# Kernel optimization log

Measured on AMD Instinct MI355X. Metric: run time of the kernel, lower is better.

Reference implementation:

```python
import jax, jax.numpy as jnp
import numpy as np

NUM_NODES = 100
WINDOW = 128
GH = 256       # graph_hidden_channels
DH = 64        # discrepancy_hidden_channels
OUT = 128      # out_channels
B = 256        # graphs per batch
N = B * NUM_NODES
E = 409600


def _mconv(x, w, b):
    # x: [B, n, W], w: [n, 2, k], b: [n, 2]  (per-node Conv1d(1,2,k), 'same' padding)
    k = w.shape[-1]
    W = x.shape[-1]
    p = k // 2
    xp = jnp.pad(x, ((0, 0), (0, 0), (p, p)))
    win = jnp.stack([xp[..., j:j + W] for j in range(k)], axis=-1)  # [B,n,W,k]
    return jnp.einsum('bnwk,nck->bncw', win, w) + b[None, :, :, None]


def _gcn(x, edge_index, Wg, bg):
    # PyG GCNConv: add self-loops, symmetric normalization, then linear
    Nn = x.shape[0]
    xw = x @ Wg.T
    loops = jnp.arange(Nn, dtype=edge_index.dtype)
    src = jnp.concatenate([edge_index[0], loops])
    dst = jnp.concatenate([edge_index[1], loops])
    deg = jax.ops.segment_sum(jnp.ones(src.shape[0], dtype=xw.dtype), dst, num_segments=Nn)
    norm = jax.lax.rsqrt(jnp.maximum(deg, 1e-12))
    coef = norm[src] * norm[dst]
    agg = jax.ops.segment_sum(coef[:, None] * xw[src], dst, num_segments=Nn)
    return agg + bg


def setup_inputs() -> dict:
    key = jax.random.key(0)
    ks = jax.random.split(key, 20)
    f = 6 * WINDOW
    s = lambda d: 1.0 / np.sqrt(d)
    inp = {
        'x1': jax.random.normal(ks[0], (N, WINDOW), jnp.float32),
        'x2': jax.random.normal(ks[1], (N, WINDOW), jnp.float32),
        'edge_index1': jax.random.randint(ks[2], (2, E), 0, N, jnp.int32),
        'edge_index2': jax.random.randint(ks[3], (2, E), 0, N, jnp.int32),
        'w3': jax.random.normal(ks[4], (NUM_NODES, 2, 3), jnp.float32) * s(3),
        'b3': jax.random.normal(ks[5], (NUM_NODES, 2), jnp.float32) * s(3),
        'w5': jax.random.normal(ks[6], (NUM_NODES, 2, 5), jnp.float32) * s(5),
        'b5': jax.random.normal(ks[7], (NUM_NODES, 2), jnp.float32) * s(5),
        'w7': jax.random.normal(ks[8], (NUM_NODES, 2, 7), jnp.float32) * s(7),
        'b7': jax.random.normal(ks[9], (NUM_NODES, 2), jnp.float32) * s(7),
        'Wff': jax.random.normal(ks[10], (NUM_NODES, GH, f), jnp.float32) * s(f),
        'bff': jax.random.normal(ks[11], (NUM_NODES, GH), jnp.float32) * s(f),
        'Wg': jax.random.normal(ks[12], (GH, GH), jnp.float32) * s(GH),
        'bg': jax.random.normal(ks[13], (GH,), jnp.float32) * s(GH),
        'Wd': jax.random.normal(ks[14], (NUM_NODES, DH, 2 * GH), jnp.float32) * s(2 * GH),
        'bd': jax.random.normal(ks[15], (NUM_NODES, DH), jnp.float32) * s(2 * GH),
        'Wfc': jax.random.normal(ks[16], (OUT, NUM_NODES * DH), jnp.float32) * s(NUM_NODES * DH),
        'bfc': jax.random.normal(ks[17], (OUT,), jnp.float32) * s(NUM_NODES * DH),
    }
    return inp


def reference(x1, x2, edge_index1, edge_index2, w3, b3, w5, b5, w7, b7,
              Wff, bff, Wg, bg, Wd, bd, Wfc, bfc):
    n = w3.shape[0]
    Nn, W = x1.shape
    Bg = Nn // n

    def branch(x):
        xg = x.reshape(Bg, n, W)
        # multiscale CNN: concat conv3/conv5/conv7 along channel -> [B,n,6,W]
        c = jnp.concatenate([_mconv(xg, w3, b3), _mconv(xg, w5, b5), _mconv(xg, w7, b7)], axis=2)
        c = jax.nn.relu(c.reshape(Bg, n, 6 * W))            # channel-major flatten (matches view(-1))
        h = jax.nn.relu(jnp.einsum('bnf,nhf->bnh', c, Wff) + bff)
        return h.reshape(Nn, -1)

    h1 = jax.nn.relu(_gcn(branch(x1), edge_index1, Wg, bg))
    h2 = jax.nn.relu(_gcn(branch(x2), edge_index2, Wg, bg))
    H = h1.shape[-1]
    cat = jnp.concatenate([h1.reshape(Bg, n, H), h2.reshape(Bg, n, H)], axis=-1)  # [B,n,2H]
    d = jnp.einsum('bnf,ndf->bnd', cat, Wd) + bd            # per-node discrepancy FC
    du = jax.nn.relu(d.reshape(Bg, -1))                     # node-major -> [B, n*DH]
    return du @ Wfc.T + bfc
```

## Files before the change

### kernel.cpp

```cpp
#include <hip/hip_runtime.h>

#define DI __device__ __forceinline__

typedef __bf16 bf16_t;
typedef bf16_t bf16x8 __attribute__((ext_vector_type(8)));
typedef float f32x4 __attribute__((ext_vector_type(4)));
typedef ushort ushort8v __attribute__((ext_vector_type(8)));

static constexpr int NNODE = 100, WIN = 128, GH = 256, DH = 64, OUTC = 128, NB = 256;
static constexpr int NTOT = NB * NNODE;
static constexpr int NE = 409600;
static constexpr int FFK = 6 * WIN;
static constexpr size_t CB = (size_t)NNODE * NB * FFK;
static constexpr size_t HB = (size_t)NTOT * GH;
static constexpr int CVT_BLKS = 4064;
static constexpr int NSEG = 64, SEGE = NE / NSEG;
static constexpr int NPK = NTOT / 2;
static constexpr int NRANGE = 4, RDST = NTOT / NRANGE;
static constexpr int RPK = RDST / 2;
static constexpr int HIST_BLKS = 2 * NSEG * NRANGE;

DI ushort f2bf(float f) {
  union { float f; unsigned u; } v; v.f = f;
  unsigned r = v.u + 0x7fffu + ((v.u >> 16) & 1u);
  return (ushort)(r >> 16);
}
DI float bf2f(ushort s) {
  union { unsigned u; float f; } v; v.u = ((unsigned)s) << 16; return v.f;
}
DI float u2f(uint u) { union { uint u; float f; } v; v.u = u; return v.f; }

DI void gload16(const void* g, void* l) {
  __builtin_amdgcn_global_load_lds((const __attribute__((address_space(1))) void*)g,
                                   (__attribute__((address_space(3))) void*)l, 16, 0, 0);
}


DI void cvt_body(int bx, const float* s0, const float* s1, const float* s2,
                 ushort* d0, ushort* d1, ushort* d2) {
  int j = bx * 256 + threadIdx.x;
  const float* s; ushort* d;
  if (j < 3276800 / 4) { s = s0; d = d0; }
  else if ((j -= 3276800 / 4) < 819200 / 4) { s = s1; d = d1; }
  else { j -= 819200 / 4; s = s2; d = d2; }
  float4 v = reinterpret_cast<const float4*>(s)[j];
  ushort4 o;
  o.x = f2bf(v.x); o.y = f2bf(v.y); o.z = f2bf(v.z); o.w = f2bf(v.w);
  reinterpret_cast<ushort4*>(d)[j] = o;
}

DI void histseg_body(int bx, const int* e1d, const int* e2d,
                     ushort* rank_local, uint* segcnt, uint* cnt ) {
  int set = bx & 1, seg = (bx >> 1) & (NSEG - 1), range = bx >> 7;
  int tid = threadIdx.x;
  for (int k = tid; k < RPK; k += 256) cnt[k] = 0;
  __syncthreads();
  const int* dstp = (set ? e2d : e1d) + seg * SEGE;
  ushort* rl = rank_local + set * NE + seg * SEGE;
  const int dbase = range * RDST;
#pragma unroll
  for (int k = 0; k < SEGE / 256; ++k) {
    int i = k * 256 + tid;
    uint dl = (uint)(dstp[i] - dbase);
    if (dl < (uint)RDST) {
      uint sh = (dl & 1) * 16;
      uint old = atomicAdd(&cnt[dl >> 1], 1u << sh);
      rl[i] = (ushort)((old >> sh) & 0xffffu);
    }
  }
  __syncthreads();
  uint* sc = segcnt + (size_t)(set * NSEG + seg) * NPK + range * RPK;
  for (int k = tid; k < RPK; k += 256) sc[k] = cnt[k];
}

DI void fill_body(int bx, const int* e1, const int* e2, const int* offs,
                  const ushort* rank_local, const uint* segbase, int* csr) {
  int i = bx * 256 + threadIdx.x;
  int set = i >= NE;
  int ii = i - set * NE;
  const int* e = set ? e2 : e1;
  int d = e[NE + ii];
  int seg = ii / SEGE;
  uint b32 = segbase[(size_t)(set * NSEG + seg) * NPK + (d >> 1)];
  int base = (b32 >> ((d & 1) * 16)) & 0xffff;
  int pos = offs[set * (NTOT + 1) + d] + base + rank_local[i];
  csr[set * NE + pos] = e[ii];
}

DI void segscan_body(int set, int pb, const uint* segcnt, uint* segbase, int* deg) {
  int p = pb * 256 + threadIdx.x;
  uint lo = 0, hi = 0;
  const uint* sc = segcnt + (size_t)set * NSEG * NPK + p;
  uint* sb = segbase + (size_t)set * NSEG * NPK + p;
  for (int s = 0; s < NSEG; ++s) {
    uint v = sc[(size_t)s * NPK];
    sb[(size_t)s * NPK] = lo | (hi << 16);
    lo += v & 0xffffu; hi += v >> 16;
  }
  reinterpret_cast<int2*>(deg)[set * NPK + p] = make_int2((int)lo, (int)hi);
}

DI void scan_body(int set, const int* deg_, int* offs_, float* norm_) {
  const int* deg = deg_ + set * NTOT;
  int* offs = offs_ + set * (NTOT + 1);
  float* norm = norm_ + set * NTOT;
  __shared__ int part[256];
  int t = threadIdx.x;
  int base = t * 100;
  int s = 0;
  for (int j = 0; j < 100; ++j) s += deg[base + j];
  part[t] = s;
  __syncthreads();
  for (int d = 1; d < 256; d <<= 1) {
    int vv = (t >= d) ? part[t - d] : 0;
    __syncthreads();
    part[t] += vv;
    __syncthreads();
  }
  int run = (t > 0) ? part[t - 1] : 0;
  for (int j = 0; j < 100; ++j) {
    int dv = deg[base + j];
    offs[base + j] = run;
    norm[base + j] = rsqrtf((float)(dv + 1));
    run += dv;
  }
  if (t == 255) offs[NTOT] = part[255];
}

DI void conv_body(int bx, const float* x1, const float* x2,
                  const float* w3, const float* b3, const float* w5, const float* b5,
                  const float* w7, const float* b7, ushort* c, float* xs ) {
  const int t = threadIdx.x;
  const int rowi = t >> 4;
  const int idx = t & 15;
  int r = bx * 16 + rowi;
  int br = r >= NTOT;
  int rr = r - br * NTOT;
  const float* x = br ? x2 : x1;
  int b = rr / 100, node = rr - b * 100;

  float* row = xs + rowi * 136;
  const int w0 = idx * 8;
  float4 v0 = *reinterpret_cast<const float4*>(x + (size_t)rr * WIN + w0);
  float4 v1 = *reinterpret_cast<const float4*>(x + (size_t)rr * WIN + w0 + 4);
  *reinterpret_cast<float4*>(&row[4 + w0]) = v0;
  *reinterpret_cast<float4*>(&row[4 + w0 + 4]) = v1;
  if (idx == 0) { row[0] = 0.f; row[1] = 0.f; row[2] = 0.f; row[3] = 0.f; }
  if (idx == 15) { row[132] = 0.f; row[133] = 0.f; row[134] = 0.f; row[135] = 0.f; }
  __syncthreads();

  float xv[14];
#pragma unroll
  for (int j = 0; j < 14; ++j) xv[j] = row[1 + w0 + j];

  const float* W3 = w3 + node * 6;  const float* B3 = b3 + node * 2;
  const float* W5 = w5 + node * 10; const float* B5 = b5 + node * 2;
  const float* W7 = w7 + node * 14; const float* B7 = b7 + node * 2;
  ushort* out = c + (size_t)br * CB + (size_t)(node * NB + b) * FFK + w0;

#pragma unroll
  for (int ch = 0; ch < 2; ++ch) {
    float k3[3], k5[5], k7[7];
#pragma unroll
    for (int j = 0; j < 3; ++j) k3[j] = W3[ch * 3 + j];
#pragma unroll
    for (int j = 0; j < 5; ++j) k5[j] = W5[ch * 5 + j];
#pragma unroll
    for (int j = 0; j < 7; ++j) k7[j] = W7[ch * 7 + j];
    float bb3 = B3[ch], bb5 = B5[ch], bb7 = B7[ch];
    ushort8v o3, o5, o7;
#pragma unroll
    for (int p = 0; p < 8; ++p) {
      float a3 = bb3, a5 = bb5, a7 = bb7;
#pragma unroll
      for (int j = 0; j < 3; ++j) a3 += k3[j] * xv[p + 2 + j];
#pragma unroll
      for (int j = 0; j < 5; ++j) a5 += k5[j] * xv[p + 1 + j];
#pragma unroll
      for (int j = 0; j < 7; ++j) a7 += k7[j] * xv[p + j];
      o3[p] = f2bf(fmaxf(a3, 0.f));
      o5[p] = f2bf(fmaxf(a5, 0.f));
      o7[p] = f2bf(fmaxf(a7, 0.f));
    }
    *reinterpret_cast<ushort8v*>(out + (0 + ch) * WIN) = o3;
    *reinterpret_cast<ushort8v*>(out + (2 + ch) * WIN) = o5;
    *reinterpret_cast<ushort8v*>(out + (4 + ch) * WIN) = o7;
  }
}

template <int MODE>
DI void gemm_body(int bx, int by, const ushort* __restrict__ A, const ushort* __restrict__ A2,
                  const ushort* __restrict__ Bm, const float* __restrict__ Bf32,
                  ushort* __restrict__ obf, float* __restrict__ of, const float* __restrict__ bias) {
  constexpr int BN = (MODE == 1 || MODE == 3) ? 128 : 64;
  constexpr int KT = (MODE == 0) ? 12 : (MODE == 1) ? 4 : (MODE == 2) ? 8 : 4;
  constexpr int LDA = (MODE == 0) ? 768 : (MODE == 1) ? 256 : (MODE == 2) ? 256 : 6400;
  constexpr int LDB = (MODE == 0) ? 768 : (MODE == 1) ? 256 : (MODE == 2) ? 512 : 6400;
  constexpr int MF = (MODE == 2) ? 2 : 4;
  constexpr int NF = (MODE == 0) ? 2 : 4;
  constexpr int NTW = (MODE == 0) ? 64 : 128;

  __shared__ ushort As[128 * 64];
  __shared__ ushort Bs[BN * 64];

  const int tid = threadIdx.x, wv = tid >> 6, lane = tid & 63;
  const int j8 = (((lane & 7) ^ (lane >> 3)) - (lane & 7)) * 8;

  int mt = 0, nt = 0, node = 0, kbase = 0, br = 0;
  if constexpr (MODE == 0) {
    int h = bx;
    int s = (h & 7) * 200 + (h >> 3);
    nt = s & 3; int rest = s >> 2;
    mt = rest & 1; int yy = rest >> 1;
    br = yy >= 100; node = yy - br * 100;
  } else if constexpr (MODE == 1) {
    int h = bx;
    int s = (h & 7) * 100 + (h >> 3);
    nt = s & 1; int rest = s >> 1;
    br = rest >= 200; mt = rest - br * 200;
  } else if constexpr (MODE == 2) { mt = bx; node = by; }
  else { mt = bx; kbase = by * 256; }

  const ushort* Ab = nullptr; const ushort* Bb = nullptr; const float* Bfp = nullptr;
  if constexpr (MODE == 0) { Ab = A + (size_t)br * CB + (size_t)node * (NB * FFK) + (size_t)mt * 128 * FFK;
                             Bfp = Bf32 + (size_t)node * (GH * FFK) + (size_t)nt * 64 * FFK; }
  else if constexpr (MODE == 1) { Ab = A + (size_t)br * HB + (size_t)mt * 128 * GH;
                                  Bb = Bm + (size_t)nt * 128 * GH; }
  else if constexpr (MODE == 2) { Bb = Bm + (size_t)node * (DH * 512); }
  else { Ab = A + (size_t)mt * 128 * 6400 + kbase; Bb = Bm + kbase; }

  const int wr = (MODE == 2) ? wv : (wv >> 1);
  const int wc = (MODE == 2) ? 0 : (wv & 1);

  f32x4 acc[MF][NF] = {};

  float4 pb[4];
  const int prow0 = (tid >> 3), pcc = tid & 7;
  if constexpr (MODE == 0) {
#pragma unroll
    for (int it = 0; it < 2; ++it) {
      const float* fp = Bfp + (size_t)(it * 32 + prow0) * LDB + 0 + pcc * 8;
      pb[it * 2]     = *reinterpret_cast<const float4*>(fp);
      pb[it * 2 + 1] = *reinterpret_cast<const float4*>(fp + 4);
    }
  }

  for (int kt = 0; kt < KT; ++kt) {
    const int k0 = kt * 64;
    __syncthreads();
#pragma unroll
    for (int it = 0; it < 4; ++it) {
      int rb = it * 32 + wv * 8;
      int row = rb + (lane >> 3);
      const ushort* gp;
      if constexpr (MODE == 2) {
        int b_ = mt * 128 + row;
        const ushort* src = (k0 < 256) ? A : A2;
        gp = src + (size_t)(b_ * NNODE + node) * GH + (k0 & 255) + (lane & 7) * 8 + j8;
      } else {
        gp = Ab + (size_t)row * LDA + k0 + (lane & 7) * 8 + j8;
      }
      gload16(gp, &As[rb * 64]);
    }
    if constexpr (MODE == 0) {
#pragma unroll
      for (int it = 0; it < 2; ++it) {
        int row = it * 32 + prow0;
        float4 v0 = pb[it * 2], v1 = pb[it * 2 + 1];
        ushort8v o;
        o[0] = f2bf(v0.x); o[1] = f2bf(v0.y); o[2] = f2bf(v0.z); o[3] = f2bf(v0.w);
        o[4] = f2bf(v1.x); o[5] = f2bf(v1.y); o[6] = f2bf(v1.z); o[7] = f2bf(v1.w);
        *reinterpret_cast<ushort8v*>(&Bs[row * 64 + ((pcc ^ (row & 7)) * 8)]) = o;
      }
    } else {
#pragma unroll
      for (int it = 0; it < BN / 32; ++it) {
        int rb = it * 32 + wv * 8;
        int row = rb + (lane >> 3);
        gload16(Bb + (size_t)row * LDB + k0 + (lane & 7) * 8 + j8, &Bs[rb * 64]);
      }
    }
    __syncthreads();
    if constexpr (MODE == 0) {
      if (kt + 1 < KT) {
        const int kn = (kt + 1) * 64;
#pragma unroll
        for (int it = 0; it < 2; ++it) {
          const float* fp = Bfp + (size_t)(it * 32 + prow0) * LDB + kn + pcc * 8;
          pb[it * 2]     = *reinterpret_cast<const float4*>(fp);
          pb[it * 2 + 1] = *reinterpret_cast<const float4*>(fp + 4);
        }
      }
    }
#pragma unroll
    for (int kk = 0; kk < 2; ++kk) {
      const int ch8 = ((kk * 4 + (lane >> 4)) ^ (lane & 7)) * 8;
      bf16x8 af[MF], bfr[NF];
#pragma unroll
      for (int m = 0; m < MF; ++m) {
        int rr = wr * (MF * 16) + m * 16 + (lane & 15);
        af[m] = *reinterpret_cast<const bf16x8*>(&As[rr * 64 + ch8]);
      }
#pragma unroll
      for (int n = 0; n < NF; ++n) {
        int rr = wc * (NF * 16) + n * 16 + (lane & 15);
        bfr[n] = *reinterpret_cast<const bf16x8*>(&Bs[rr * 64 + ch8]);
      }
#pragma unroll
      for (int m = 0; m < MF; ++m)
#pragma unroll
        for (int n = 0; n < NF; ++n)
          acc[m][n] = __builtin_amdgcn_mfma_f32_16x16x32_bf16(af[m], bfr[n], acc[m][n], 0, 0, 0);
    }
  }

  const int lrow = (lane >> 4) * 4, lcol = lane & 15;
#pragma unroll
  for (int m = 0; m < MF; ++m) {
#pragma unroll
    for (int n = 0; n < NF; ++n) {
      int cc = wc * (NF * 16) + n * 16 + lcol;
#pragma unroll
      for (int rg = 0; rg < 4; ++rg) {
        int rr = wr * (MF * 16) + m * 16 + lrow + rg;
        float val = acc[m][n][rg];
        if constexpr (MODE == 0) {
          int b_ = mt * 128 + rr;
          int col = nt * NTW + cc;
          val = fmaxf(val + bias[node * GH + col], 0.f);
          obf[(size_t)br * HB + (size_t)(b_ * NNODE + node) * GH + col] = f2bf(val);
        } else if constexpr (MODE == 1) {
          int R = mt * 128 + rr;
          int col = nt * 128 + cc;
          obf[(size_t)br * HB + (size_t)R * GH + col] = f2bf(val * bias[br * NTOT + R]);
        } else if constexpr (MODE == 2) {
          int b_ = mt * 128 + rr;
          val = fmaxf(val + bias[node * DH + cc], 0.f);
          obf[(size_t)b_ * (NNODE * DH) + node * DH + cc] = f2bf(val);
        } else {
          int R = mt * 128 + rr;
          if (by == 0) val += bias[cc];
          atomicAdd(&of[R * OUTC + cc], val);
        }
      }
    }
  }
}


__global__ __launch_bounds__(256) void fused1_k(
    const float* __restrict__ Wd, const float* __restrict__ Wfc, const float* __restrict__ Wg,
    ushort* __restrict__ Wdb, ushort* __restrict__ Wfcb, ushort* __restrict__ Wgb,
    const int* __restrict__ e1d, const int* __restrict__ e2d,
    ushort* __restrict__ rank_local, uint* __restrict__ segcnt,
    const float* __restrict__ x1, const float* __restrict__ x2,
    const float* __restrict__ w3, const float* __restrict__ b3,
    const float* __restrict__ w5, const float* __restrict__ b5,
    const float* __restrict__ w7, const float* __restrict__ b7,
    ushort* __restrict__ c) {
  __shared__ uint smem[RPK];
  int bx = blockIdx.x;
  if (bx < HIST_BLKS) histseg_body(bx, e1d, e2d, rank_local, segcnt, smem);
  else if (bx < HIST_BLKS + 3200) conv_body(bx - HIST_BLKS, x1, x2, w3, b3, w5, b5, w7, b7, c, (float*)smem);
  else cvt_body(bx - HIST_BLKS - 3200, Wd, Wfc, Wg, Wdb, Wfcb, Wgb);
}

__global__ __launch_bounds__(256) void fused3_k(
    const ushort* __restrict__ cbuf, const float* __restrict__ Wff,
    ushort* __restrict__ h, const float* __restrict__ bff,
    const uint* __restrict__ segcnt, uint* __restrict__ segbase, int* __restrict__ deg) {
  if ((int)blockIdx.x < 1600)
    gemm_body<0>(blockIdx.x, 0, cbuf, nullptr, nullptr, Wff, h, nullptr, bff);
  else {
    int b = blockIdx.x - 1600;
    segscan_body(b / 50, b % 50, segcnt, segbase, deg);
  }
}

__global__ __launch_bounds__(256) void scan_k(const int* __restrict__ deg,
                                              int* __restrict__ offs, float* __restrict__ nrm) {
  scan_body(blockIdx.x, deg, offs, nrm);
}

__global__ __launch_bounds__(256) void fused4_k(
    const ushort* __restrict__ h, const ushort* __restrict__ Wgb,
    ushort* __restrict__ xw, const float* __restrict__ nrm,
    const int* __restrict__ e1, const int* __restrict__ e2,
    const int* __restrict__ offs, const ushort* __restrict__ rank_local,
    const uint* __restrict__ segbase, int* __restrict__ csr) {
  if ((int)blockIdx.x < 800)
    gemm_body<1>(blockIdx.x, 0, h, nullptr, Wgb, nullptr, xw, nullptr, nrm);
  else
    fill_body(blockIdx.x - 800, e1, e2, offs, rank_local, segbase, csr);
}

template <int MODE>
__global__ __launch_bounds__(256) void gemm_k(const ushort* __restrict__ A, const ushort* __restrict__ A2,
                                              const ushort* __restrict__ Bm, ushort* __restrict__ obf,
                                              float* __restrict__ of, const float* __restrict__ bias) {
  gemm_body<MODE>(blockIdx.x, blockIdx.y, A, A2, Bm, nullptr, obf, of, bias);
}

__global__ __launch_bounds__(256) void agg_k(const ushort* __restrict__ xw_, const int* __restrict__ offs_,
                                             const int* __restrict__ csr_, const float* __restrict__ norm_,
                                             const float* __restrict__ bg, ushort* __restrict__ hg_) {
  int bid = blockIdx.x;
  int c = bid & 7;
  int i = bid >> 3;
  int br = c >> 2, slice = c & 3;
  int g = threadIdx.x >> 3;
  int v = i * 32 + g;
  int l8 = threadIdx.x & 7;
  int col = slice * 64 + l8 * 8;

  const ushort* xw = xw_ + (size_t)br * HB;
  const int* offs = offs_ + br * (NTOT + 1);
  const int* csr = csr_ + br * NE;
  const float* norm = norm_ + br * NTOT;
  ushort* hg = hg_ + (size_t)br * HB;
  const uint* base = reinterpret_cast<const uint*>(xw + col);

  float a[8];
  {
    uint4 q = *reinterpret_cast<const uint4*>(base + (size_t)v * (GH / 2));
    a[0] = u2f(q.x << 16); a[1] = u2f(q.x & 0xffff0000u);
    a[2] = u2f(q.y << 16); a[3] = u2f(q.y & 0xffff0000u);
    a[4] = u2f(q.z << 16); a[5] = u2f(q.z & 0xffff0000u);
    a[6] = u2f(q.w << 16); a[7] = u2f(q.w & 0xffff0000u);
  }
  int e0 = offs[v], e1v = offs[v + 1];
  int j = e0;
  for (; j + 1 < e1v; j += 2) {
    int s0 = csr[j], s1 = csr[j + 1];
    uint4 q0 = *reinterpret_cast<const uint4*>(base + (size_t)s0 * (GH / 2));
    uint4 q1 = *reinterpret_cast<const uint4*>(base + (size_t)s1 * (GH / 2));
    a[0] += u2f(q0.x << 16) + u2f(q1.x << 16);
    a[1] += u2f(q0.x & 0xffff0000u) + u2f(q1.x & 0xffff0000u);
    a[2] += u2f(q0.y << 16) + u2f(q1.y << 16);
    a[3] += u2f(q0.y & 0xffff0000u) + u2f(q1.y & 0xffff0000u);
    a[4] += u2f(q0.z << 16) + u2f(q1.z << 16);
    a[5] += u2f(q0.z & 0xffff0000u) + u2f(q1.z & 0xffff0000u);
    a[6] += u2f(q0.w << 16) + u2f(q1.w << 16);
    a[7] += u2f(q0.w & 0xffff0000u) + u2f(q1.w & 0xffff0000u);
  }
  if (j < e1v) {
    int s0 = csr[j];
    uint4 q0 = *reinterpret_cast<const uint4*>(base + (size_t)s0 * (GH / 2));
    a[0] += u2f(q0.x << 16); a[1] += u2f(q0.x & 0xffff0000u);
    a[2] += u2f(q0.y << 16); a[3] += u2f(q0.y & 0xffff0000u);
    a[4] += u2f(q0.z << 16); a[5] += u2f(q0.z & 0xffff0000u);
    a[6] += u2f(q0.w << 16); a[7] += u2f(q0.w & 0xffff0000u);
  }

  float nv = norm[v];
  float4 bb0 = *reinterpret_cast<const float4*>(bg + col);
  float4 bb1 = *reinterpret_cast<const float4*>(bg + col + 4);
  ushort8v o;
  o[0] = f2bf(fmaxf(nv * a[0] + bb0.x, 0.f));
  o[1] = f2bf(fmaxf(nv * a[1] + bb0.y, 0.f));
  o[2] = f2bf(fmaxf(nv * a[2] + bb0.z, 0.f));
  o[3] = f2bf(fmaxf(nv * a[3] + bb0.w, 0.f));
  o[4] = f2bf(fmaxf(nv * a[4] + bb1.x, 0.f));
  o[5] = f2bf(fmaxf(nv * a[5] + bb1.y, 0.f));
  o[6] = f2bf(fmaxf(nv * a[6] + bb1.z, 0.f));
  o[7] = f2bf(fmaxf(nv * a[7] + bb1.w, 0.f));
  *reinterpret_cast<ushort8v*>(hg + (size_t)v * GH + col) = o;
}

extern "C" void kernel_launch(void* const* d_in, const int* in_sizes, int n_in,
                              void* d_out, int out_size, void* d_ws, size_t ws_size,
                              hipStream_t stream) {
  const float* x1 = (const float*)d_in[0];
  const float* x2 = (const float*)d_in[1];
  const int* e1 = (const int*)d_in[2];
  const int* e2 = (const int*)d_in[3];
  const float* w3 = (const float*)d_in[4];  const float* b3 = (const float*)d_in[5];
  const float* w5 = (const float*)d_in[6];  const float* b5 = (const float*)d_in[7];
  const float* w7 = (const float*)d_in[8];  const float* b7 = (const float*)d_in[9];
  const float* Wff = (const float*)d_in[10]; const float* bff = (const float*)d_in[11];
  const float* Wg = (const float*)d_in[12];  const float* bg = (const float*)d_in[13];
  const float* Wd = (const float*)d_in[14];  const float* bd = (const float*)d_in[15];
  const float* Wfc = (const float*)d_in[16]; const float* bfc = (const float*)d_in[17];
  float* out = (float*)d_out;

  char* ws = (char*)d_ws;
  size_t off = 0;
  auto alloc = [&](size_t bytes) -> char* {
    char* p = ws + off;
    off = (off + bytes + 255) & ~(size_t)255;
    return p;
  };
  ushort* Wdb  = (ushort*)alloc(3276800ull * 2);
  ushort* Wfcb = (ushort*)alloc(819200ull * 2);
  ushort* Wgb  = (ushort*)alloc(65536ull * 2);
  ushort* cbuf = (ushort*)alloc(2 * CB * 2);
  ushort* h    = (ushort*)alloc(2 * HB * 2);
  ushort* xw   = (ushort*)alloc(2 * HB * 2);
  int* deg     = (int*)alloc(2 * NTOT * 4);
  int* offs    = (int*)alloc(2 * (NTOT + 1) * 4);
  ushort* rankl = (ushort*)alloc(2 * NE * 2);
  uint* segcnt  = (uint*)alloc((size_t)2 * NSEG * NPK * 4);
  uint* segbase = (uint*)alloc((size_t)2 * NSEG * NPK * 4);
  int* csr     = (int*)alloc(2 * NE * 4);
  float* nrm   = (float*)alloc(2 * NTOT * 4);
  ushort* du = cbuf;

  hipMemsetAsync(out, 0, (size_t)out_size * 4, stream);

  fused1_k<<<HIST_BLKS + 3200 + CVT_BLKS, 256, 0, stream>>>(
      Wd, Wfc, Wg, Wdb, Wfcb, Wgb,
      e1 + NE, e2 + NE, rankl, segcnt,
      x1, x2, w3, b3, w5, b5, w7, b7, cbuf);
  fused3_k<<<1700, 256, 0, stream>>>(cbuf, Wff, h, bff, segcnt, segbase, deg);
  scan_k<<<2, 256, 0, stream>>>(deg, offs, nrm);
  fused4_k<<<4000, 256, 0, stream>>>(h, Wgb, xw, nrm, e1, e2, offs, rankl, segbase, csr);

  agg_k<<<6400, 256, 0, stream>>>(xw, offs, csr, nrm, bg, h);

  gemm_k<2><<<dim3(2, 100), 256, 0, stream>>>(h, h + HB, Wdb, du, nullptr, bd);
  gemm_k<3><<<dim3(2, 25), 256, 0, stream>>>(du, nullptr, Wfcb, nullptr, out, bfc);
}
```

Measured before the change: 225.5 us.

## Stage fp32 Wff tiles directly into LDS and convert to bf16 at fragment load

In the per-node FF GEMM, the fp32 weight tile is no longer register-prefetched and converted to bf16 before the LDS store. It is now copied straight into a doubled-size, XOR-swizzled fp32 LDS buffer with async global-to-LDS loads. Each B fragment is converted to bf16 at read time, and launch bounds request 4 blocks per CU. This removes the register staging and the serial conversion step, at the cost of more LDS per block, more LDS read traffic, and repeated conversion work for each wave's fragment reads.

```diff
diff --git a/kernel.cpp b/kernel.cpp
--- a/kernel.cpp
+++ b/kernel.cpp
@@ -199,9 +199,10 @@
   constexpr int MF = (MODE == 2) ? 2 : 4;
   constexpr int NF = (MODE == 0) ? 2 : 4;
   constexpr int NTW = (MODE == 0) ? 64 : 128;
+  constexpr int BSE = (MODE == 0) ? 64 * 64 * 2 : BN * 64;
 
   __shared__ ushort As[128 * 64];
-  __shared__ ushort Bs[BN * 64];
+  __shared__ ushort Bs[BSE];
 
   const int tid = threadIdx.x, wv = tid >> 6, lane = tid & 63;
   const int j8 = (((lane & 7) ^ (lane >> 3)) - (lane & 7)) * 8;
@@ -234,17 +235,6 @@
 
   f32x4 acc[MF][NF] = {};
 
-  float4 pb[4];
-  const int prow0 = (tid >> 3), pcc = tid & 7;
-  if constexpr (MODE == 0) {
-#pragma unroll
-    for (int it = 0; it < 2; ++it) {
-      const float* fp = Bfp + (size_t)(it * 32 + prow0) * LDB + 0 + pcc * 8;
-      pb[it * 2]     = *reinterpret_cast<const float4*>(fp);
-      pb[it * 2 + 1] = *reinterpret_cast<const float4*>(fp + 4);
-    }
-  }
-
   for (int kt = 0; kt < KT; ++kt) {
     const int k0 = kt * 64;
     __syncthreads();
@@ -263,14 +253,13 @@
       gload16(gp, &As[rb * 64]);
     }
     if constexpr (MODE == 0) {
-#pragma unroll
-      for (int it = 0; it < 2; ++it) {
-        int row = it * 32 + prow0;
-        float4 v0 = pb[it * 2], v1 = pb[it * 2 + 1];
-        ushort8v o;
-        o[0] = f2bf(v0.x); o[1] = f2bf(v0.y); o[2] = f2bf(v0.z); o[3] = f2bf(v0.w);
-        o[4] = f2bf(v1.x); o[5] = f2bf(v1.y); o[6] = f2bf(v1.z); o[7] = f2bf(v1.w);
-        *reinterpret_cast<ushort8v*>(&Bs[row * 64 + ((pcc ^ (row & 7)) * 8)]) = o;
+      float* Bf = reinterpret_cast<float*>(Bs);
+#pragma unroll
+      for (int it = 0; it < 4; ++it) {
+        int seg = wv * 4 + it;
+        int row = seg * 4 + (lane >> 4);
+        int tc = (lane & 15) ^ (row & 15);
+        gload16(Bfp + (size_t)row * LDB + k0 + tc * 4, &Bf[seg * 256]);
       }
     } else {
 #pragma unroll
@@ -281,17 +270,6 @@
       }
     }
     __syncthreads();
-    if constexpr (MODE == 0) {
-      if (kt + 1 < KT) {
-        const int kn = (kt + 1) * 64;
-#pragma unroll
-        for (int it = 0; it < 2; ++it) {
-          const float* fp = Bfp + (size_t)(it * 32 + prow0) * LDB + kn + pcc * 8;
-          pb[it * 2]     = *reinterpret_cast<const float4*>(fp);
-          pb[it * 2 + 1] = *reinterpret_cast<const float4*>(fp + 4);
-        }
-      }
-    }
 #pragma unroll
     for (int kk = 0; kk < 2; ++kk) {
       const int ch8 = ((kk * 4 + (lane >> 4)) ^ (lane & 7)) * 8;
@@ -303,8 +281,21 @@
       }
 #pragma unroll
       for (int n = 0; n < NF; ++n) {
-        int rr = wc * (NF * 16) + n * 16 + (lane & 15);
-        bfr[n] = *reinterpret_cast<const bf16x8*>(&Bs[rr * 64 + ch8]);
+        if constexpr (MODE == 0) {
+          const float* Bf = reinterpret_cast<const float*>(Bs);
+          int rr = wc * 32 + n * 16 + (lane & 15);
+          int tc = kk * 8 + (lane >> 4) * 2;
+          int key = rr & 15;
+          f32x4 q0 = *reinterpret_cast<const f32x4*>(&Bf[rr * 64 + ((tc ^ key) * 4)]);
+          f32x4 q1 = *reinterpret_cast<const f32x4*>(&Bf[rr * 64 + (((tc + 1) ^ key) * 4)]);
+          bf16x8 f;
+          f[0] = (bf16_t)q0[0]; f[1] = (bf16_t)q0[1]; f[2] = (bf16_t)q0[2]; f[3] = (bf16_t)q0[3];
+          f[4] = (bf16_t)q1[0]; f[5] = (bf16_t)q1[1]; f[6] = (bf16_t)q1[2]; f[7] = (bf16_t)q1[3];
+          bfr[n] = f;
+        } else {
+          int rr = wc * (NF * 16) + n * 16 + (lane & 15);
+          bfr[n] = *reinterpret_cast<const bf16x8*>(&Bs[rr * 64 + ch8]);
+        }
       }
 #pragma unroll
       for (int m = 0; m < MF; ++m)
@@ -365,7 +356,7 @@
   else cvt_body(bx - HIST_BLKS - 3200, Wd, Wfc, Wg, Wdb, Wfcb, Wgb);
 }
 
-__global__ __launch_bounds__(256) void fused3_k(
+__global__ __launch_bounds__(256, 4) void fused3_k(
     const ushort* __restrict__ cbuf, const float* __restrict__ Wff,
     ushort* __restrict__ h, const float* __restrict__ bff,
     const uint* __restrict__ segcnt, uint* __restrict__ segbase, int* __restrict__ deg) {
```

Result: no change. 225.1 us (-0.2%).
